# Optimization experiments

Hardware: AMD Instinct MI355X
Metric: run time of the kernel (lower is better)

## Reference

```python
import jax, jax.numpy as jnp
import numpy as np

OUT_F = 4096   # compressed rows; logical m = 2*OUT_F
IN_F = 2048    # compressed cols; logical k = 2*IN_F
BATCH = 4096   # n = input.shape[0]

# valid sorted 2-of-4 column patterns for 2:4 structured sparsity
_PAIR_LUT = jnp.array([[0, 1], [0, 2], [0, 3], [1, 2], [1, 3], [2, 3]], dtype=jnp.int32)


def setup_inputs() -> dict:
    key = jax.random.key(0)
    k1, k2, k3, k4 = jax.random.split(key, 4)
    weight = jax.random.normal(k1, (OUT_F, IN_F), dtype=jnp.float32)
    # vector (row) sparsity: keep 1 of every 2 logical row-vectors -> collision-free logical row ids
    row_bit = jax.random.randint(k2, (OUT_F,), 0, 2)
    indices = (2 * jnp.arange(OUT_F, dtype=jnp.int32) + row_bit.astype(jnp.int32))
    # 2:4 column sparsity: per group of 4 logical cols, keep 2 distinct sorted positions
    pat = jax.random.randint(k3, (OUT_F, IN_F // 2), 0, 6)
    metadata = _PAIR_LUT[pat].reshape(OUT_F, IN_F)  # [OUT_F, IN_F], values in 0..3
    inp = jax.random.normal(k4, (BATCH, 2 * IN_F), dtype=jnp.float32)
    return {"weight": weight, "indices": indices, "metadata": metadata, "input": inp}


def reference(weight, indices, metadata, input):
    # Decompress the dual structured-sparse weight to its logical dense form,
    # then compute W_logical @ input^T (spmm_dense_trans semantics).
    out_f, in_f = weight.shape
    m, k = 2 * out_f, 2 * in_f
    # logical column of each compressed element: group base 4*(c//2) + 2-bit metadata
    col = 4 * (jnp.arange(in_f, dtype=jnp.int32) // 2)[None, :] + metadata  # [out_f, in_f]
    W = jnp.zeros((m, k), dtype=weight.dtype).at[indices[:, None], col].set(weight)
    return W @ input.T  # [m, n] = [2*out_f, batch]
```

## Files before the change

kernel.cpp:

```cpp
#include <hip/hip_runtime.h>

#define OUT_F 4096
#define IN_F  2048
#define KLOG  4096
#define NB    4096
typedef unsigned long long ull;
typedef ull ullx2 __attribute__((ext_vector_type(2)));

typedef __bf16 bf16x8 __attribute__((ext_vector_type(8)));
typedef short  s16x8  __attribute__((ext_vector_type(8)));
typedef float  f32x4  __attribute__((ext_vector_type(4)));
typedef float  f32x16 __attribute__((ext_vector_type(16)));

__device__ __forceinline__ unsigned short f2bf(float f) {
    unsigned int u = __float_as_uint(f);
    u += 0x7fffu + ((u >> 16) & 1u);
    return (unsigned short)(u >> 16);
}

__device__ __forceinline__ void gload_lds16(const void* g, void* l) {
    __builtin_amdgcn_global_load_lds(
        (const __attribute__((address_space(1))) unsigned int*)g,
        (__attribute__((address_space(3))) unsigned int*)l, 16, 0, 0);
}

__device__ __forceinline__ bf16x8 ldsf(const char* p) {
    return __builtin_bit_cast(bf16x8, *(const s16x8*)p);
}

#define MFMA32(a, b, c) __builtin_amdgcn_mfma_f32_32x32x16_bf16((a), (b), (c), 0, 0, 0)

__global__ __launch_bounds__(256) void prep_kernel(
    const float* __restrict__ weight, const int* __restrict__ metadata,
    const float* __restrict__ input,
    unsigned short* __restrict__ wsA, unsigned short* __restrict__ wsB)
{
    const int b = blockIdx.x;
    if (b < 4096) {
        const int g = b * 256 + threadIdx.x;
        const int r = g >> 8;
        const int c = (g & 255) * 8;
        const size_t off = (size_t)r * IN_F + c;
        const float4 w0 = *(const float4*)(weight + off);
        const float4 w1 = *(const float4*)(weight + off + 4);
        const int4   m0 = *(const int4*)(metadata + off);
        const int4   m1 = *(const int4*)(metadata + off + 4);
        ullx2 v01, v23;
        v01.x = ((ull)f2bf(w0.x) << (m0.x * 16)) | ((ull)f2bf(w0.y) << (m0.y * 16));
        v01.y = ((ull)f2bf(w0.z) << (m0.z * 16)) | ((ull)f2bf(w0.w) << (m0.w * 16));
        v23.x = ((ull)f2bf(w1.x) << (m1.x * 16)) | ((ull)f2bf(w1.y) << (m1.y * 16));
        v23.y = ((ull)f2bf(w1.z) << (m1.z * 16)) | ((ull)f2bf(w1.w) << (m1.w * 16));
        ull* dst = (ull*)(wsA + (size_t)r * KLOG + 2 * c);
        *(ullx2*)(dst)     = v01;
        *(ullx2*)(dst + 2) = v23;
    } else {
        const int g = (b - 4096) * 256 + threadIdx.x;
        const size_t off = (size_t)g * 16;
        const float4 f0 = *(const float4*)(input + off);
        const float4 f1 = *(const float4*)(input + off + 4);
        const float4 f2 = *(const float4*)(input + off + 8);
        const float4 f3 = *(const float4*)(input + off + 12);
        ullx2 v01, v23;
        v01.x =  (ull)f2bf(f0.x) | ((ull)f2bf(f0.y) << 16) | ((ull)f2bf(f0.z) << 32) | ((ull)f2bf(f0.w) << 48);
        v01.y =  (ull)f2bf(f1.x) | ((ull)f2bf(f1.y) << 16) | ((ull)f2bf(f1.z) << 32) | ((ull)f2bf(f1.w) << 48);
        v23.x =  (ull)f2bf(f2.x) | ((ull)f2bf(f2.y) << 16) | ((ull)f2bf(f2.z) << 32) | ((ull)f2bf(f2.w) << 48);
        v23.y =  (ull)f2bf(f3.x) | ((ull)f2bf(f3.y) << 16) | ((ull)f2bf(f3.z) << 32) | ((ull)f2bf(f3.w) << 48);
        ull* dst = (ull*)(wsB + off);
        *(ullx2*)(dst)     = v01;
        *(ullx2*)(dst + 2) = v23;
    }
}

__global__ __launch_bounds__(512, 2) void gemm_kernel256(
    const unsigned short* __restrict__ wsA, const unsigned short* __restrict__ wsB,
    const int* __restrict__ indices, float* __restrict__ out)
{
    __shared__ __align__(16) char lds[4 * 32768];

    const int tid  = threadIdx.x;
    const int lane = tid & 63;
    const int wave = tid >> 6;
    const int wm   = wave >> 2;
    const int wn   = wave & 3;
    const int l31  = lane & 31;
    const int h    = lane >> 5;

    const int swz = ((blockIdx.x & 7) << 5) | (blockIdx.x >> 3);
    const int r0 = (swz >> 4) << 8;
    const int b0 = (swz & 15) << 8;

    const int srow   = tid >> 2;
    const int schunk = (tid & 3) ^ ((tid >> 3) & 3);
    const unsigned short* gA = wsA + (size_t)(r0 + srow) * KLOG + schunk * 8;
    const unsigned short* gB = wsB + (size_t)(b0 + srow) * KLOG + schunk * 8;
    char* const ldsW = lds + wave * 1024;

    const int q = (l31 >> 1) & 3;
    const unsigned x0 = (unsigned)(((0 + h) ^ q) * 16);
    const unsigned x1 = (unsigned)(((2 + h) ^ q) * 16);
    const unsigned aRow = (unsigned)((wm * 128 + l31) * 64);
    const unsigned bRow = (unsigned)((wn * 64  + l31) * 64);

    f32x16 acc[4][2];
#pragma unroll
    for (int i = 0; i < 4; ++i)
#pragma unroll
        for (int j = 0; j < 2; ++j)
#pragma unroll
            for (int e = 0; e < 16; ++e) acc[i][j][e] = 0.f;

#define STAGE_A(t_) do { \
        char* _d = ldsW + (((t_) & 3) * 32768); \
        const unsigned short* _s = gA + (t_) * 32; \
        gload_lds16(_s, _d); \
        gload_lds16(_s + (size_t)128 * KLOG, _d + 8192); } while (0)
#define STAGE_B(t_) do { \
        char* _d = ldsW + (((t_) & 3) * 32768) + 16384; \
        const unsigned short* _s = gB + (t_) * 32; \
        gload_lds16(_s, _d); \
        gload_lds16(_s + (size_t)128 * KLOG, _d + 8192); } while (0)

    STAGE_A(0); STAGE_B(0);
    STAGE_A(1); STAGE_B(1);
    STAGE_A(2); STAGE_B(2);
    asm volatile("s_waitcnt vmcnt(8)" ::: "memory");
    __builtin_amdgcn_s_barrier();
    __builtin_amdgcn_sched_barrier(0);

    for (int t = 0; t < 128; ++t) {
        const unsigned bufA = (unsigned)(t & 3) * 32768u;
        const char* pA = lds + bufA + aRow;
        const char* pB = lds + bufA + 16384u + bRow;

        bf16x8 a00 = ldsf(pA + x0);
        bf16x8 b00 = ldsf(pB + x0);
        bf16x8 b10 = ldsf(pB + 2048 + x0);
        bf16x8 a10 = ldsf(pA + 2048 + x0);
        bf16x8 a20 = ldsf(pA + 4096 + x0);
        bf16x8 a30 = ldsf(pA + 6144 + x0);
        bf16x8 a01 = ldsf(pA + x1);
        bf16x8 b01 = ldsf(pB + x1);
        bf16x8 b11 = ldsf(pB + 2048 + x1);
        bf16x8 a11 = ldsf(pA + 2048 + x1);
        bf16x8 a21 = ldsf(pA + 4096 + x1);
        bf16x8 a31 = ldsf(pA + 6144 + x1);
        if (t < 125) { STAGE_A(t + 3); STAGE_B(t + 3); }

        __builtin_amdgcn_s_setprio(1);
        acc[0][0] = MFMA32(a00, b00, acc[0][0]);
        acc[0][1] = MFMA32(a00, b10, acc[0][1]);
        acc[1][0] = MFMA32(a10, b00, acc[1][0]);
        acc[1][1] = MFMA32(a10, b10, acc[1][1]);
        acc[2][0] = MFMA32(a20, b00, acc[2][0]);
        acc[2][1] = MFMA32(a20, b10, acc[2][1]);
        acc[3][0] = MFMA32(a30, b00, acc[3][0]);
        acc[3][1] = MFMA32(a30, b10, acc[3][1]);
        acc[0][0] = MFMA32(a01, b01, acc[0][0]);
        acc[0][1] = MFMA32(a01, b11, acc[0][1]);
        acc[1][0] = MFMA32(a11, b01, acc[1][0]);
        acc[1][1] = MFMA32(a11, b11, acc[1][1]);
        acc[2][0] = MFMA32(a21, b01, acc[2][0]);
        acc[2][1] = MFMA32(a21, b11, acc[2][1]);
        acc[3][0] = MFMA32(a31, b01, acc[3][0]);
        acc[3][1] = MFMA32(a31, b11, acc[3][1]);
        __builtin_amdgcn_s_setprio(0);

        if (t < 125) {
            asm volatile("s_waitcnt vmcnt(8)" ::: "memory");
        } else if (t == 125) {
            asm volatile("s_waitcnt vmcnt(4)" ::: "memory");
        } else if (t == 126) {
            asm volatile("s_waitcnt vmcnt(0)" ::: "memory");
        }
        __builtin_amdgcn_s_barrier();
        __builtin_amdgcn_sched_barrier(0);
    }
#undef STAGE_A
#undef STAGE_B

#pragma unroll
    for (int fm = 0; fm < 4; ++fm) {
#pragma unroll
        for (int reg = 0; reg < 16; ++reg) {
            const int rloc = wm * 128 + fm * 32 + (reg & 3) + 8 * (reg >> 2) + 4 * h;
            const int L = indices[r0 + rloc];
            const size_t base  = (size_t)L * NB;
            const size_t baseZ = (size_t)(L ^ 1) * NB;
#pragma unroll
            for (int fn = 0; fn < 2; ++fn) {
                const int col = b0 + wn * 64 + fn * 32 + l31;
                out[base  + col] = acc[fm][fn][reg];
                out[baseZ + col] = 0.0f;
            }
        }
    }
}

__global__ __launch_bounds__(256) void spmm_dt_fallback(
    const float* __restrict__ weight, const int* __restrict__ indices,
    const int* __restrict__ metadata, const float* __restrict__ input,
    float* __restrict__ out)
{
    __shared__ __align__(16) unsigned short As[128][32];
    __shared__ __align__(16) unsigned short Bs[128][32];
    const int tid = threadIdx.x, lane = tid & 63, wave = tid >> 6;
    const int wm = wave >> 1, wn = wave & 1, l15 = lane & 15, quad = lane >> 4;
    const int r0 = blockIdx.y * 128, b0 = blockIdx.x * 128;
    f32x4 acc[4][4];
#pragma unroll
    for (int i = 0; i < 4; ++i)
#pragma unroll
        for (int j = 0; j < 4; ++j) acc[i][j] = (f32x4){0.f, 0.f, 0.f, 0.f};
    const int srow = tid >> 3, sgrp = tid & 7;
    for (int kk = 0; kk < KLOG / 32; ++kk) {
        const int c0 = kk * 16, k0 = kk * 32;
#pragma unroll
        for (int s = 0; s < 4; ++s) {
            const int row = srow + s * 32;
            const size_t off = (size_t)(r0 + row) * IN_F + c0 + 2 * sgrp;
            const float2 w = *(const float2*)(weight + off);
            const int2  md = *(const int2*)(metadata + off);
            *(ull*)(&As[row][4 * sgrp]) =
                ((ull)f2bf(w.x) << (md.x * 16)) | ((ull)f2bf(w.y) << (md.y * 16));
        }
#pragma unroll
        for (int s = 0; s < 4; ++s) {
            const int row = srow + s * 32;
            const float4 f = *(const float4*)(&input[(size_t)(b0 + row) * KLOG + k0 + sgrp * 4]);
            *(ull*)(&Bs[row][sgrp * 4]) =
                 (ull)f2bf(f.x) | ((ull)f2bf(f.y) << 16) |
                ((ull)f2bf(f.z) << 32) | ((ull)f2bf(f.w) << 48);
        }
        __syncthreads();
        bf16x8 a[4], b[4];
#pragma unroll
        for (int i = 0; i < 4; ++i)
            a[i] = __builtin_bit_cast(bf16x8, *(const s16x8*)(&As[wm * 64 + i * 16 + l15][quad * 8]));
#pragma unroll
        for (int j = 0; j < 4; ++j)
            b[j] = __builtin_bit_cast(bf16x8, *(const s16x8*)(&Bs[wn * 64 + j * 16 + l15][quad * 8]));
#pragma unroll
        for (int i = 0; i < 4; ++i)
#pragma unroll
            for (int j = 0; j < 4; ++j)
                acc[i][j] = __builtin_amdgcn_mfma_f32_16x16x32_bf16(a[i], b[j], acc[i][j], 0, 0, 0);
        __syncthreads();
    }
#pragma unroll
    for (int i = 0; i < 4; ++i)
#pragma unroll
        for (int t = 0; t < 4; ++t) {
            const int r = r0 + wm * 64 + i * 16 + quad * 4 + t;
            const int L = indices[r];
            const size_t base = (size_t)L * NB, baseZ = (size_t)(L ^ 1) * NB;
#pragma unroll
            for (int j = 0; j < 4; ++j) {
                const int col = b0 + wn * 64 + j * 16 + l15;
                out[base + col] = acc[i][j][t];
                out[baseZ + col] = 0.0f;
            }
        }
}

extern "C" void kernel_launch(void* const* d_in, const int* in_sizes, int n_in,
                              void* d_out, int out_size, void* d_ws, size_t ws_size,
                              hipStream_t stream) {
    const float* weight   = (const float*)d_in[0];
    const int*   indices  = (const int*)d_in[1];
    const int*   metadata = (const int*)d_in[2];
    const float* input    = (const float*)d_in[3];
    float*       out      = (float*)d_out;

    const size_t needA = (size_t)OUT_F * KLOG * 2;
    const size_t needB = (size_t)NB * KLOG * 2;
    if (ws_size >= needA + needB) {
        unsigned short* wsA = (unsigned short*)d_ws;
        unsigned short* wsB = wsA + (size_t)OUT_F * KLOG;
        prep_kernel<<<dim3(8192), dim3(256), 0, stream>>>(weight, metadata, input, wsA, wsB);
        gemm_kernel256<<<dim3(256), dim3(512), 0, stream>>>(wsA, wsB, indices, out);
    } else {
        spmm_dt_fallback<<<dim3(NB / 128, OUT_F / 128), dim3(256), 0, stream>>>(
            weight, indices, metadata, input, out);
    }
}
```

Baseline: 376.3 us.

## Split GEMM k-step into two barrier-synchronized phases interleaving LDS reads and MFMA

```diff
diff --git a/kernel.cpp b/kernel.cpp
--- a/kernel.cpp
+++ b/kernel.cpp
@@ -120,63 +120,125 @@
         gload_lds16(_s, _d); \
         gload_lds16(_s + (size_t)128 * KLOG, _d + 8192); } while (0)
 
+#define BAR()      __builtin_amdgcn_s_barrier()
+#define SCHED0()   __builtin_amdgcn_sched_barrier(0)
+#define LGKM0()    asm volatile("s_waitcnt lgkmcnt(0)" ::: "memory")
+
     STAGE_A(0); STAGE_B(0);
     STAGE_A(1); STAGE_B(1);
     STAGE_A(2); STAGE_B(2);
     asm volatile("s_waitcnt vmcnt(8)" ::: "memory");
-    __builtin_amdgcn_s_barrier();
-    __builtin_amdgcn_sched_barrier(0);
-
-    for (int t = 0; t < 128; ++t) {
-        const unsigned bufA = (unsigned)(t & 3) * 32768u;
-        const char* pA = lds + bufA + aRow;
-        const char* pB = lds + bufA + 16384u + bRow;
-
-        bf16x8 a00 = ldsf(pA + x0);
-        bf16x8 b00 = ldsf(pB + x0);
-        bf16x8 b10 = ldsf(pB + 2048 + x0);
-        bf16x8 a10 = ldsf(pA + 2048 + x0);
-        bf16x8 a20 = ldsf(pA + 4096 + x0);
-        bf16x8 a30 = ldsf(pA + 6144 + x0);
-        bf16x8 a01 = ldsf(pA + x1);
-        bf16x8 b01 = ldsf(pB + x1);
-        bf16x8 b11 = ldsf(pB + 2048 + x1);
-        bf16x8 a11 = ldsf(pA + 2048 + x1);
-        bf16x8 a21 = ldsf(pA + 4096 + x1);
-        bf16x8 a31 = ldsf(pA + 6144 + x1);
-        if (t < 125) { STAGE_A(t + 3); STAGE_B(t + 3); }
-
+    BAR();
+    SCHED0();
+
+    for (int i = 0; i < 64; ++i) {
+        const int ta = 2 * i, tb = 2 * i + 1;
+        const char* pAa = lds + (unsigned)(ta & 3) * 32768u + aRow;
+        const char* pBa = lds + (unsigned)(ta & 3) * 32768u + 16384u + bRow;
+        const char* pAb = lds + (unsigned)(tb & 3) * 32768u + aRow;
+        const char* pBb = lds + (unsigned)(tb & 3) * 32768u + 16384u + bRow;
+
+        bf16x8 b00 = ldsf(pBa + x0);
+        bf16x8 b10 = ldsf(pBa + 2048 + x0);
+        bf16x8 b01 = ldsf(pBa + x1);
+        bf16x8 b11 = ldsf(pBa + 2048 + x1);
+        bf16x8 a00 = ldsf(pAa + x0);
+        bf16x8 a01 = ldsf(pAa + x1);
+        bf16x8 a10 = ldsf(pAa + 2048 + x0);
+        bf16x8 a11 = ldsf(pAa + 2048 + x1);
+        if (i <= 62) STAGE_A(ta + 3);
+        BAR();
+        LGKM0();
+        SCHED0();
         __builtin_amdgcn_s_setprio(1);
         acc[0][0] = MFMA32(a00, b00, acc[0][0]);
         acc[0][1] = MFMA32(a00, b10, acc[0][1]);
         acc[1][0] = MFMA32(a10, b00, acc[1][0]);
         acc[1][1] = MFMA32(a10, b10, acc[1][1]);
+        acc[0][0] = MFMA32(a01, b01, acc[0][0]);
+        acc[0][1] = MFMA32(a01, b11, acc[0][1]);
+        acc[1][0] = MFMA32(a11, b01, acc[1][0]);
+        acc[1][1] = MFMA32(a11, b11, acc[1][1]);
+        __builtin_amdgcn_s_setprio(0);
+        BAR();
+        SCHED0();
+
+        bf16x8 a20 = ldsf(pAa + 4096 + x0);
+        bf16x8 a21 = ldsf(pAa + 4096 + x1);
+        bf16x8 a30 = ldsf(pAa + 6144 + x0);
+        bf16x8 a31 = ldsf(pAa + 6144 + x1);
+        if (i <= 62) STAGE_B(ta + 3);
+        BAR();
+        LGKM0();
+        SCHED0();
+        __builtin_amdgcn_s_setprio(1);
         acc[2][0] = MFMA32(a20, b00, acc[2][0]);
         acc[2][1] = MFMA32(a20, b10, acc[2][1]);
         acc[3][0] = MFMA32(a30, b00, acc[3][0]);
         acc[3][1] = MFMA32(a30, b10, acc[3][1]);
-        acc[0][0] = MFMA32(a01, b01, acc[0][0]);
-        acc[0][1] = MFMA32(a01, b11, acc[0][1]);
-        acc[1][0] = MFMA32(a11, b01, acc[1][0]);
-        acc[1][1] = MFMA32(a11, b11, acc[1][1]);
         acc[2][0] = MFMA32(a21, b01, acc[2][0]);
         acc[2][1] = MFMA32(a21, b11, acc[2][1]);
         acc[3][0] = MFMA32(a31, b01, acc[3][0]);
         acc[3][1] = MFMA32(a31, b11, acc[3][1]);
         __builtin_amdgcn_s_setprio(0);
-
-        if (t < 125) {
-            asm volatile("s_waitcnt vmcnt(8)" ::: "memory");
-        } else if (t == 125) {
-            asm volatile("s_waitcnt vmcnt(4)" ::: "memory");
-        } else if (t == 126) {
-            asm volatile("s_waitcnt vmcnt(0)" ::: "memory");
-        }
-        __builtin_amdgcn_s_barrier();
-        __builtin_amdgcn_sched_barrier(0);
+        if (i < 63) { asm volatile("s_waitcnt vmcnt(8)" ::: "memory"); }
+        else        { asm volatile("s_waitcnt vmcnt(0)" ::: "memory"); }
+        BAR();
+        SCHED0();
+
+        b00 = ldsf(pBb + x0);
+        b10 = ldsf(pBb + 2048 + x0);
+        b01 = ldsf(pBb + x1);
+        b11 = ldsf(pBb + 2048 + x1);
+        a00 = ldsf(pAb + x0);
+        a01 = ldsf(pAb + x1);
+        a10 = ldsf(pAb + 2048 + x0);
+        a11 = ldsf(pAb + 2048 + x1);
+        if (i <= 61) STAGE_A(tb + 3);
+        BAR();
+        LGKM0();
+        SCHED0();
+        __builtin_amdgcn_s_setprio(1);
+        acc[0][0] = MFMA32(a00, b00, acc[0][0]);
+        acc[0][1] = MFMA32(a00, b10, acc[0][1]);
+        acc[1][0] = MFMA32(a10, b00, acc[1][0]);
+        acc[1][1] = MFMA32(a10, b10, acc[1][1]);
+        acc[0][0] = MFMA32(a01, b01, acc[0][0]);
+        acc[0][1] = MFMA32(a01, b11, acc[0][1]);
+        acc[1][0] = MFMA32(a11, b01, acc[1][0]);
+        acc[1][1] = MFMA32(a11, b11, acc[1][1]);
+        __builtin_amdgcn_s_setprio(0);
+        BAR();
+        SCHED0();
+
+        a20 = ldsf(pAb + 4096 + x0);
+        a21 = ldsf(pAb + 4096 + x1);
+        a30 = ldsf(pAb + 6144 + x0);
+        a31 = ldsf(pAb + 6144 + x1);
+        if (i <= 61) STAGE_B(tb + 3);
+        BAR();
+        LGKM0();
+        SCHED0();
+        __builtin_amdgcn_s_setprio(1);
+        acc[2][0] = MFMA32(a20, b00, acc[2][0]);
+        acc[2][1] = MFMA32(a20, b10, acc[2][1]);
+        acc[3][0] = MFMA32(a30, b00, acc[3][0]);
+        acc[3][1] = MFMA32(a30, b10, acc[3][1]);
+        acc[2][0] = MFMA32(a21, b01, acc[2][0]);
+        acc[2][1] = MFMA32(a21, b11, acc[2][1]);
+        acc[3][0] = MFMA32(a31, b01, acc[3][0]);
+        acc[3][1] = MFMA32(a31, b11, acc[3][1]);
+        __builtin_amdgcn_s_setprio(0);
+        if (i <= 61)      { asm volatile("s_waitcnt vmcnt(8)" ::: "memory"); }
+        else if (i == 62) { asm volatile("s_waitcnt vmcnt(4)" ::: "memory"); }
+        BAR();
+        SCHED0();
     }
 #undef STAGE_A
 #undef STAGE_B
+#undef BAR
+#undef SCHED0
+#undef LGKM0
 
 #pragma unroll
     for (int fm = 0; fm < 4; ++fm) {
```

Measured after the change: 362.5 us. 1.04x faster.

## Software-pipeline LDS fragment reads one K-step ahead of MFMAs

Applied to the files above, without the earlier changes.

```diff
diff --git a/kernel.cpp b/kernel.cpp
--- a/kernel.cpp
+++ b/kernel.cpp
@@ -109,6 +109,9 @@
 #pragma unroll
             for (int e = 0; e < 16; ++e) acc[i][j][e] = 0.f;
 
+    bf16x8 pf0[8], pf1[8];
+    bf16x8 k1_0, k1_1, k1_2, k1_3;
+
 #define STAGE_A(t_) do { \
         char* _d = ldsW + (((t_) & 3) * 32768); \
         const unsigned short* _s = gA + (t_) * 32; \
@@ -120,63 +123,134 @@
         gload_lds16(_s, _d); \
         gload_lds16(_s + (size_t)128 * KLOG, _d + 8192); } while (0)
 
+#define BAR()     __builtin_amdgcn_s_barrier()
+#define SCHED0()  __builtin_amdgcn_sched_barrier(0)
+#define LGKM(n_)  asm volatile("s_waitcnt lgkmcnt(" #n_ ")" ::: "memory")
+#define VMC(n_)   asm volatile("s_waitcnt vmcnt(" #n_ ")" ::: "memory")
+
+#define READS(t_, NXT) do { \
+        const char* pA1 = lds + (unsigned)((t_) & 3) * 32768u + aRow; \
+        k1_0 = ldsf(pA1 + x1); \
+        k1_1 = ldsf(pA1 + 2048 + x1); \
+        k1_2 = ldsf(pA1 + 4096 + x1); \
+        k1_3 = ldsf(pA1 + 6144 + x1); \
+        const unsigned bO = (unsigned)(((t_) + 1) & 3) * 32768u; \
+        const char* pB = lds + bO + 16384u + bRow; \
+        const char* pA = lds + bO + aRow; \
+        NXT[0] = ldsf(pB + x0); \
+        NXT[1] = ldsf(pB + 2048 + x0); \
+        NXT[2] = ldsf(pB + x1); \
+        NXT[3] = ldsf(pB + 2048 + x1); \
+        NXT[4] = ldsf(pA + x0); \
+        NXT[5] = ldsf(pA + 2048 + x0); \
+        NXT[6] = ldsf(pA + 4096 + x0); \
+        NXT[7] = ldsf(pA + 6144 + x0); } while (0)
+
+#define MFMAS_K0(CUR) \
+        acc[0][0] = MFMA32(CUR[4], CUR[0], acc[0][0]); \
+        acc[0][1] = MFMA32(CUR[4], CUR[1], acc[0][1]); \
+        acc[1][0] = MFMA32(CUR[5], CUR[0], acc[1][0]); \
+        acc[1][1] = MFMA32(CUR[5], CUR[1], acc[1][1]); \
+        acc[2][0] = MFMA32(CUR[6], CUR[0], acc[2][0]); \
+        acc[2][1] = MFMA32(CUR[6], CUR[1], acc[2][1]); \
+        acc[3][0] = MFMA32(CUR[7], CUR[0], acc[3][0]); \
+        acc[3][1] = MFMA32(CUR[7], CUR[1], acc[3][1]);
+
+#define MFMAS_K1(CUR) \
+        acc[0][0] = MFMA32(k1_0, CUR[2], acc[0][0]); \
+        acc[0][1] = MFMA32(k1_0, CUR[3], acc[0][1]); \
+        acc[1][0] = MFMA32(k1_1, CUR[2], acc[1][0]); \
+        acc[1][1] = MFMA32(k1_1, CUR[3], acc[1][1]); \
+        acc[2][0] = MFMA32(k1_2, CUR[2], acc[2][0]); \
+        acc[2][1] = MFMA32(k1_2, CUR[3], acc[2][1]); \
+        acc[3][0] = MFMA32(k1_3, CUR[2], acc[3][0]); \
+        acc[3][1] = MFMA32(k1_3, CUR[3], acc[3][1]);
+
     STAGE_A(0); STAGE_B(0);
     STAGE_A(1); STAGE_B(1);
     STAGE_A(2); STAGE_B(2);
-    asm volatile("s_waitcnt vmcnt(8)" ::: "memory");
-    __builtin_amdgcn_s_barrier();
-    __builtin_amdgcn_sched_barrier(0);
-
-    for (int t = 0; t < 128; ++t) {
-        const unsigned bufA = (unsigned)(t & 3) * 32768u;
-        const char* pA = lds + bufA + aRow;
-        const char* pB = lds + bufA + 16384u + bRow;
-
-        bf16x8 a00 = ldsf(pA + x0);
-        bf16x8 b00 = ldsf(pB + x0);
-        bf16x8 b10 = ldsf(pB + 2048 + x0);
-        bf16x8 a10 = ldsf(pA + 2048 + x0);
-        bf16x8 a20 = ldsf(pA + 4096 + x0);
-        bf16x8 a30 = ldsf(pA + 6144 + x0);
-        bf16x8 a01 = ldsf(pA + x1);
-        bf16x8 b01 = ldsf(pB + x1);
-        bf16x8 b11 = ldsf(pB + 2048 + x1);
-        bf16x8 a11 = ldsf(pA + 2048 + x1);
-        bf16x8 a21 = ldsf(pA + 4096 + x1);
-        bf16x8 a31 = ldsf(pA + 6144 + x1);
-        if (t < 125) { STAGE_A(t + 3); STAGE_B(t + 3); }
-
+    VMC(4);
+    BAR();
+    SCHED0();
+    {
+        const char* pB = lds + 16384u + bRow;
+        const char* pA = lds + aRow;
+        pf0[0] = ldsf(pB + x0);
+        pf0[1] = ldsf(pB + 2048 + x0);
+        pf0[2] = ldsf(pB + x1);
+        pf0[3] = ldsf(pB + 2048 + x1);
+        pf0[4] = ldsf(pA + x0);
+        pf0[5] = ldsf(pA + 2048 + x0);
+        pf0[6] = ldsf(pA + 4096 + x0);
+        pf0[7] = ldsf(pA + 6144 + x0);
+    }
+
+    for (int i = 0; i < 63; ++i) {
+        const int ta = 2 * i, tb = 2 * i + 1;
+
+        READS(ta, pf1);
+        STAGE_A(ta + 3); STAGE_B(ta + 3);
+        SCHED0();
+        LGKM(12); SCHED0();
         __builtin_amdgcn_s_setprio(1);
-        acc[0][0] = MFMA32(a00, b00, acc[0][0]);
-        acc[0][1] = MFMA32(a00, b10, acc[0][1]);
-        acc[1][0] = MFMA32(a10, b00, acc[1][0]);
-        acc[1][1] = MFMA32(a10, b10, acc[1][1]);
-        acc[2][0] = MFMA32(a20, b00, acc[2][0]);
-        acc[2][1] = MFMA32(a20, b10, acc[2][1]);
-        acc[3][0] = MFMA32(a30, b00, acc[3][0]);
-        acc[3][1] = MFMA32(a30, b10, acc[3][1]);
-        acc[0][0] = MFMA32(a01, b01, acc[0][0]);
-        acc[0][1] = MFMA32(a01, b11, acc[0][1]);
-        acc[1][0] = MFMA32(a11, b01, acc[1][0]);
-        acc[1][1] = MFMA32(a11, b11, acc[1][1]);
-        acc[2][0] = MFMA32(a21, b01, acc[2][0]);
-        acc[2][1] = MFMA32(a21, b11, acc[2][1]);
-        acc[3][0] = MFMA32(a31, b01, acc[3][0]);
-        acc[3][1] = MFMA32(a31, b11, acc[3][1]);
+        MFMAS_K0(pf0)
+        LGKM(8); SCHED0();
+        MFMAS_K1(pf0)
         __builtin_amdgcn_s_setprio(0);
-
-        if (t < 125) {
-            asm volatile("s_waitcnt vmcnt(8)" ::: "memory");
-        } else if (t == 125) {
-            asm volatile("s_waitcnt vmcnt(4)" ::: "memory");
-        } else if (t == 126) {
-            asm volatile("s_waitcnt vmcnt(0)" ::: "memory");
-        }
-        __builtin_amdgcn_s_barrier();
-        __builtin_amdgcn_sched_barrier(0);
-    }
+        VMC(4);
+        BAR();
+        SCHED0();
+
+        READS(tb, pf0);
+        if (tb <= 124) { STAGE_A(tb + 3); STAGE_B(tb + 3); }
+        SCHED0();
+        LGKM(12); SCHED0();
+        __builtin_amdgcn_s_setprio(1);
+        MFMAS_K0(pf1)
+        LGKM(8); SCHED0();
+        MFMAS_K1(pf1)
+        __builtin_amdgcn_s_setprio(0);
+        if (tb <= 124) { VMC(4); }
+        else           { VMC(0); }
+        BAR();
+        SCHED0();
+    }
+
+    READS(126, pf1);
+    SCHED0();
+    LGKM(12); SCHED0();
+    __builtin_amdgcn_s_setprio(1);
+    MFMAS_K0(pf0)
+    LGKM(8); SCHED0();
+    MFMAS_K1(pf0)
+    __builtin_amdgcn_s_setprio(0);
+    BAR();
+    SCHED0();
+
+    {
+        const char* pA1 = lds + (unsigned)(127 & 3) * 32768u + aRow;
+        k1_0 = ldsf(pA1 + x1);
+        k1_1 = ldsf(pA1 + 2048 + x1);
+        k1_2 = ldsf(pA1 + 4096 + x1);
+        k1_3 = ldsf(pA1 + 6144 + x1);
+    }
+    SCHED0();
+    LGKM(4); SCHED0();
+    __builtin_amdgcn_s_setprio(1);
+    MFMAS_K0(pf1)
+    LGKM(0); SCHED0();
+    MFMAS_K1(pf1)
+    __builtin_amdgcn_s_setprio(0);
+
 #undef STAGE_A
 #undef STAGE_B
+#undef BAR
+#undef SCHED0
+#undef LGKM
+#undef VMC
+#undef READS
+#undef MFMAS_K0
+#undef MFMAS_K1
 
 #pragma unroll
     for (int fm = 0; fm < 4; ++fm) {
```

Result: faster. 357.2 us (-5.1%).

## Switch GEMM to 16x16x32 MFMA with split-phase loads and staging

Applied to the files above, without the earlier changes.

```diff
diff --git a/kernel.cpp b/kernel.cpp
--- a/kernel.cpp
+++ b/kernel.cpp
@@ -10,7 +10,6 @@
 typedef __bf16 bf16x8 __attribute__((ext_vector_type(8)));
 typedef short  s16x8  __attribute__((ext_vector_type(8)));
 typedef float  f32x4  __attribute__((ext_vector_type(4)));
-typedef float  f32x16 __attribute__((ext_vector_type(16)));
 
 __device__ __forceinline__ unsigned short f2bf(float f) {
     unsigned int u = __float_as_uint(f);
@@ -28,7 +27,7 @@
     return __builtin_bit_cast(bf16x8, *(const s16x8*)p);
 }
 
-#define MFMA32(a, b, c) __builtin_amdgcn_mfma_f32_32x32x16_bf16((a), (b), (c), 0, 0, 0)
+#define MFMA16(a, b, c) __builtin_amdgcn_mfma_f32_16x16x32_bf16((a), (b), (c), 0, 0, 0)
 
 __global__ __launch_bounds__(256) void prep_kernel(
     const float* __restrict__ weight, const int* __restrict__ metadata,
@@ -82,8 +81,8 @@
     const int wave = tid >> 6;
     const int wm   = wave >> 2;
     const int wn   = wave & 3;
-    const int l31  = lane & 31;
-    const int h    = lane >> 5;
+    const int l15  = lane & 15;
+    const int quad = lane >> 4;
 
     const int swz = ((blockIdx.x & 7) << 5) | (blockIdx.x >> 3);
     const int r0 = (swz >> 4) << 8;
@@ -95,19 +94,15 @@
     const unsigned short* gB = wsB + (size_t)(b0 + srow) * KLOG + schunk * 8;
     char* const ldsW = lds + wave * 1024;
 
-    const int q = (l31 >> 1) & 3;
-    const unsigned x0 = (unsigned)(((0 + h) ^ q) * 16);
-    const unsigned x1 = (unsigned)(((2 + h) ^ q) * 16);
-    const unsigned aRow = (unsigned)((wm * 128 + l31) * 64);
-    const unsigned bRow = (unsigned)((wn * 64  + l31) * 64);
-
-    f32x16 acc[4][2];
-#pragma unroll
-    for (int i = 0; i < 4; ++i)
-#pragma unroll
-        for (int j = 0; j < 2; ++j)
-#pragma unroll
-            for (int e = 0; e < 16; ++e) acc[i][j][e] = 0.f;
+    const unsigned xq    = (unsigned)((quad ^ ((l15 >> 1) & 3)) * 16);
+    const unsigned aBase = (unsigned)((wm * 128 + l15) * 64);
+    const unsigned bBase = (unsigned)((wn * 64  + l15) * 64);
+
+    f32x4 acc[8][4];
+#pragma unroll
+    for (int i = 0; i < 8; ++i)
+#pragma unroll
+        for (int j = 0; j < 4; ++j) acc[i][j] = (f32x4){0.f, 0.f, 0.f, 0.f};
 
 #define STAGE_A(t_) do { \
         char* _d = ldsW + (((t_) & 3) * 32768); \
@@ -120,49 +115,80 @@
         gload_lds16(_s, _d); \
         gload_lds16(_s + (size_t)128 * KLOG, _d + 8192); } while (0)
 
+#define BAR()     __builtin_amdgcn_s_barrier()
+#define SCHED0()  __builtin_amdgcn_sched_barrier(0)
+#define LGKM0()   asm volatile("s_waitcnt lgkmcnt(0)" ::: "memory")
+
     STAGE_A(0); STAGE_B(0);
     STAGE_A(1); STAGE_B(1);
     STAGE_A(2); STAGE_B(2);
     asm volatile("s_waitcnt vmcnt(8)" ::: "memory");
-    __builtin_amdgcn_s_barrier();
-    __builtin_amdgcn_sched_barrier(0);
+    BAR();
+    SCHED0();
 
     for (int t = 0; t < 128; ++t) {
-        const unsigned bufA = (unsigned)(t & 3) * 32768u;
-        const char* pA = lds + bufA + aRow;
-        const char* pB = lds + bufA + 16384u + bRow;
-
-        bf16x8 a00 = ldsf(pA + x0);
-        bf16x8 b00 = ldsf(pB + x0);
-        bf16x8 b10 = ldsf(pB + 2048 + x0);
-        bf16x8 a10 = ldsf(pA + 2048 + x0);
-        bf16x8 a20 = ldsf(pA + 4096 + x0);
-        bf16x8 a30 = ldsf(pA + 6144 + x0);
-        bf16x8 a01 = ldsf(pA + x1);
-        bf16x8 b01 = ldsf(pB + x1);
-        bf16x8 b11 = ldsf(pB + 2048 + x1);
-        bf16x8 a11 = ldsf(pA + 2048 + x1);
-        bf16x8 a21 = ldsf(pA + 4096 + x1);
-        bf16x8 a31 = ldsf(pA + 6144 + x1);
-        if (t < 125) { STAGE_A(t + 3); STAGE_B(t + 3); }
-
+        const unsigned bufO = (unsigned)(t & 3) * 32768u;
+        const char* pA = lds + bufO + aBase;
+        const char* pB = lds + bufO + 16384u + bBase;
+
+        bf16x8 b0f = ldsf(pB + xq);
+        bf16x8 b1f = ldsf(pB + 1024 + xq);
+        bf16x8 b2f = ldsf(pB + 2048 + xq);
+        bf16x8 b3f = ldsf(pB + 3072 + xq);
+        bf16x8 a0 = ldsf(pA + xq);
+        bf16x8 a1 = ldsf(pA + 1024 + xq);
+        bf16x8 a2 = ldsf(pA + 2048 + xq);
+        bf16x8 a3 = ldsf(pA + 3072 + xq);
+        if (t < 125) STAGE_A(t + 3);
+        BAR();
+        LGKM0();
+        SCHED0();
         __builtin_amdgcn_s_setprio(1);
-        acc[0][0] = MFMA32(a00, b00, acc[0][0]);
-        acc[0][1] = MFMA32(a00, b10, acc[0][1]);
-        acc[1][0] = MFMA32(a10, b00, acc[1][0]);
-        acc[1][1] = MFMA32(a10, b10, acc[1][1]);
-        acc[2][0] = MFMA32(a20, b00, acc[2][0]);
-        acc[2][1] = MFMA32(a20, b10, acc[2][1]);
-        acc[3][0] = MFMA32(a30, b00, acc[3][0]);
-        acc[3][1] = MFMA32(a30, b10, acc[3][1]);
-        acc[0][0] = MFMA32(a01, b01, acc[0][0]);
-        acc[0][1] = MFMA32(a01, b11, acc[0][1]);
-        acc[1][0] = MFMA32(a11, b01, acc[1][0]);
-        acc[1][1] = MFMA32(a11, b11, acc[1][1]);
-        acc[2][0] = MFMA32(a21, b01, acc[2][0]);
-        acc[2][1] = MFMA32(a21, b11, acc[2][1]);
-        acc[3][0] = MFMA32(a31, b01, acc[3][0]);
-        acc[3][1] = MFMA32(a31, b11, acc[3][1]);
+        acc[0][0] = MFMA16(a0, b0f, acc[0][0]);
+        acc[0][1] = MFMA16(a0, b1f, acc[0][1]);
+        acc[0][2] = MFMA16(a0, b2f, acc[0][2]);
+        acc[0][3] = MFMA16(a0, b3f, acc[0][3]);
+        acc[1][0] = MFMA16(a1, b0f, acc[1][0]);
+        acc[1][1] = MFMA16(a1, b1f, acc[1][1]);
+        acc[1][2] = MFMA16(a1, b2f, acc[1][2]);
+        acc[1][3] = MFMA16(a1, b3f, acc[1][3]);
+        acc[2][0] = MFMA16(a2, b0f, acc[2][0]);
+        acc[2][1] = MFMA16(a2, b1f, acc[2][1]);
+        acc[2][2] = MFMA16(a2, b2f, acc[2][2]);
+        acc[2][3] = MFMA16(a2, b3f, acc[2][3]);
+        acc[3][0] = MFMA16(a3, b0f, acc[3][0]);
+        acc[3][1] = MFMA16(a3, b1f, acc[3][1]);
+        acc[3][2] = MFMA16(a3, b2f, acc[3][2]);
+        acc[3][3] = MFMA16(a3, b3f, acc[3][3]);
+        __builtin_amdgcn_s_setprio(0);
+        BAR();
+        SCHED0();
+
+        bf16x8 a4 = ldsf(pA + 4096 + xq);
+        bf16x8 a5 = ldsf(pA + 5120 + xq);
+        bf16x8 a6 = ldsf(pA + 6144 + xq);
+        bf16x8 a7 = ldsf(pA + 7168 + xq);
+        if (t < 125) STAGE_B(t + 3);
+        BAR();
+        LGKM0();
+        SCHED0();
+        __builtin_amdgcn_s_setprio(1);
+        acc[4][0] = MFMA16(a4, b0f, acc[4][0]);
+        acc[4][1] = MFMA16(a4, b1f, acc[4][1]);
+        acc[4][2] = MFMA16(a4, b2f, acc[4][2]);
+        acc[4][3] = MFMA16(a4, b3f, acc[4][3]);
+        acc[5][0] = MFMA16(a5, b0f, acc[5][0]);
+        acc[5][1] = MFMA16(a5, b1f, acc[5][1]);
+        acc[5][2] = MFMA16(a5, b2f, acc[5][2]);
+        acc[5][3] = MFMA16(a5, b3f, acc[5][3]);
+        acc[6][0] = MFMA16(a6, b0f, acc[6][0]);
+        acc[6][1] = MFMA16(a6, b1f, acc[6][1]);
+        acc[6][2] = MFMA16(a6, b2f, acc[6][2]);
+        acc[6][3] = MFMA16(a6, b3f, acc[6][3]);
+        acc[7][0] = MFMA16(a7, b0f, acc[7][0]);
+        acc[7][1] = MFMA16(a7, b1f, acc[7][1]);
+        acc[7][2] = MFMA16(a7, b2f, acc[7][2]);
+        acc[7][3] = MFMA16(a7, b3f, acc[7][3]);
         __builtin_amdgcn_s_setprio(0);
 
         if (t < 125) {
@@ -172,24 +198,27 @@
         } else if (t == 126) {
             asm volatile("s_waitcnt vmcnt(0)" ::: "memory");
         }
-        __builtin_amdgcn_s_barrier();
-        __builtin_amdgcn_sched_barrier(0);
+        BAR();
+        SCHED0();
     }
 #undef STAGE_A
 #undef STAGE_B
-
-#pragma unroll
-    for (int fm = 0; fm < 4; ++fm) {
-#pragma unroll
-        for (int reg = 0; reg < 16; ++reg) {
-            const int rloc = wm * 128 + fm * 32 + (reg & 3) + 8 * (reg >> 2) + 4 * h;
+#undef BAR
+#undef SCHED0
+#undef LGKM0
+
+#pragma unroll
+    for (int rg = 0; rg < 8; ++rg) {
+#pragma unroll
+        for (int e = 0; e < 4; ++e) {
+            const int rloc = wm * 128 + rg * 16 + quad * 4 + e;
             const int L = indices[r0 + rloc];
             const size_t base  = (size_t)L * NB;
             const size_t baseZ = (size_t)(L ^ 1) * NB;
 #pragma unroll
-            for (int fn = 0; fn < 2; ++fn) {
-                const int col = b0 + wn * 64 + fn * 32 + l31;
-                out[base  + col] = acc[fm][fn][reg];
+            for (int cf = 0; cf < 4; ++cf) {
+                const int col = b0 + wn * 64 + cf * 16 + l15;
+                out[base  + col] = acc[rg][cf][e];
                 out[baseZ + col] = 0.0f;
             }
         }
```

Measured after the change: 354.3 us. -5.8%, faster.
